# Kernel tuning notes

Measured on AMD Instinct MI355X. Metric: run time of the kernel, lower is better.

The kernel has to match this reference:

```python
import jax, jax.numpy as jnp
import numpy as np

GAMMA = 0.99
GAE_LAMBDA = 0.95
CLIP = 0.2
ENT_COEF = 0.01
VF_COEF = 0.5


def setup_inputs() -> dict:
    key = jax.random.key(0)
    ks = jax.random.split(key, 12)
    T, D, H, A = 65536, 512, 256, 16
    obs = jax.random.normal(ks[0], (T, D), dtype=jnp.float32)
    actions = jax.random.randint(ks[1], (T,), 0, A, dtype=jnp.int32)
    logprobs = jax.random.normal(ks[2], (T,), dtype=jnp.float32)
    rewards = jax.random.normal(ks[3], (T,), dtype=jnp.float32)
    terms = jax.random.uniform(ks[4], (T,), dtype=jnp.float32)
    values = jax.random.normal(ks[5], (T,), dtype=jnp.float32)
    # orthogonal-init-like scaling (std sqrt(2) for trunk, 0.01 actor, 1.0 critic)
    W1 = jax.random.normal(ks[6], (D, H), dtype=jnp.float32) * np.float32(np.sqrt(2.0 / D))
    b1 = jnp.zeros((H,), jnp.float32)
    W2 = jax.random.normal(ks[7], (H, H), dtype=jnp.float32) * np.float32(np.sqrt(2.0 / H))
    b2 = jnp.zeros((H,), jnp.float32)
    Wa = jax.random.normal(ks[8], (H, A), dtype=jnp.float32) * np.float32(0.01 / np.sqrt(H))
    ba = jnp.zeros((A,), jnp.float32)
    Wc = jax.random.normal(ks[9], (H, 1), dtype=jnp.float32) * np.float32(1.0 / np.sqrt(H))
    bc = jnp.zeros((1,), jnp.float32)
    return {"obs": obs, "actions": actions, "logprobs": logprobs, "rewards": rewards,
            "terms": terms, "values": values, "W1": W1, "b1": b1, "W2": W2, "b2": b2,
            "Wa": Wa, "ba": ba, "Wc": Wc, "bc": bc}


def reference(obs, actions, logprobs, rewards, terms, values,
              W1, b1, W2, b2, Wa, ba, Wc, bc):
    # ---- GAE (torch.no_grad in original -> stop_gradient) ----
    nonterm = 1.0 - terms                                   # [T]
    next_vals = jnp.concatenate([values[1:], jnp.zeros((1,), values.dtype)])
    delta = rewards + GAMMA * next_vals * nonterm - values  # [T]

    def step(carry, x):  # reverse recurrence a_t = d_t + g*l*nt_t * a_{t+1}
        d, nt = x
        g = d + GAMMA * GAE_LAMBDA * nt * carry
        return g, g

    _, adv = jax.lax.scan(step, jnp.float32(0.0), (delta, nonterm), reverse=True)
    adv = jax.lax.stop_gradient(adv)
    returns = adv + jax.lax.stop_gradient(values)
    vals_old = jax.lax.stop_gradient(values)

    # ---- actor-critic MLP (get_action_and_value) ----
    hidden = jnp.tanh(jnp.tanh(obs @ W1 + b1) @ W2 + b2)    # [T,256]
    logits = hidden @ Wa + ba                               # [T,A]
    logp = jax.nn.log_softmax(logits, axis=-1)
    newlp = jnp.take_along_axis(logp, actions[:, None].astype(jnp.int32), axis=1)[:, 0]
    entropy = -jnp.sum(jnp.exp(logp) * logp, axis=-1)       # [T]
    value = (hidden @ Wc + bc)[:, 0]                        # [T]

    # ---- clipped PPO losses (single full-batch minibatch) ----
    ratio = jnp.exp(newlp - logprobs)
    a = (adv - adv.mean()) / (adv.std() + 1e-8)
    pg_loss = jnp.maximum(-a * ratio, -a * jnp.clip(ratio, 1.0 - CLIP, 1.0 + CLIP)).mean()
    v_clipped = vals_old + jnp.clip(value - vals_old, -CLIP, CLIP)
    v_loss = 0.5 * jnp.maximum((value - returns) ** 2, (v_clipped - returns) ** 2).mean()
    loss = pg_loss - ENT_COEF * entropy.mean() + VF_COEF * v_loss
    return loss
```

## Files before the change

### kernel.cpp

```cpp
#include <hip/hip_runtime.h>


#define TT 65536

typedef float f32x4 __attribute__((ext_vector_type(4)));
typedef __bf16 bf16x8 __attribute__((ext_vector_type(8)));
typedef unsigned short u16x8 __attribute__((ext_vector_type(8)));
typedef unsigned int u32x4 __attribute__((ext_vector_type(4)));

__device__ __forceinline__ unsigned short f2bf(float f) {
    unsigned int u = __float_as_uint(f);
    unsigned int r = (u + 0x7fffu + ((u >> 16) & 1u)) >> 16;
    return (unsigned short)r;
}

__device__ __forceinline__ unsigned int cvt_pk_bf16(float a, float b) {
    unsigned int r;
    asm("v_cvt_pk_bf16_f32 %0, %1, %2" : "=v"(r) : "v"(a), "v"(b));
    return r;
}

__device__ __forceinline__ float fast_tanh(float x) {
    float e = __expf(2.0f * x);
    return fmaf(-2.0f, __builtin_amdgcn_rcpf(e + 1.0f), 1.0f);
}

__device__ __forceinline__ void lds_barrier() {
    asm volatile("s_waitcnt lgkmcnt(0)" ::: "memory");
    __builtin_amdgcn_s_barrier();
}

__device__ __forceinline__ void suffix_scan256(float* sC, float* sD, int i) {
    float c = sC[i], d = sD[i];
#pragma unroll
    for (int s = 1; s < 256; s <<= 1) {
        float c2 = 1.0f, d2 = 0.0f;
        if (i + s < 256) { c2 = sC[i + s]; d2 = sD[i + s]; }
        __syncthreads();
        d = d + c * d2;
        c = c * c2;
        sC[i] = c; sD[i] = d;
        __syncthreads();
    }
}

__device__ __forceinline__ void gae_cd(const float* rewards, const float* terms,
                                       const float* values, int t, float* c, float* d) {
    float nt = 1.0f - terms[t];
    float nv = (t + 1 < TT) ? values[t + 1] : 0.0f;
    *d = rewards[t] + 0.99f * nv * nt - values[t];
    *c = 0.99f * 0.95f * nt;
}

__global__ void k_prep_gae1(const float* __restrict__ W1, const float* __restrict__ W2,
                            const float* __restrict__ Wa, const float* __restrict__ Wc,
                            unsigned short* __restrict__ W1Tf, unsigned short* __restrict__ W2Tf,
                            unsigned short* __restrict__ Wavf,
                            const float* __restrict__ rewards, const float* __restrict__ terms,
                            const float* __restrict__ values, float* __restrict__ aggC,
                            float* __restrict__ aggD) {
    if (blockIdx.x < 800) {
        int idx = blockIdx.x * 256 + threadIdx.x;
        if (idx < 131072) {
            int col = idx & 255, k = idx >> 8;
            int kt = k >> 5, lh = (k & 31) >> 3, e = k & 7;
            int nt = col >> 4, cl = col & 15;
            W1Tf[(((kt * 16 + nt) * 64) + lh * 16 + cl) * 8 + e] = f2bf(W1[k * 256 + col]);
        } else if (idx < 196608) {
            int i = idx - 131072;
            int col = i & 255, k = i >> 8;
            int kt = k >> 5, lh = (k & 31) >> 3, e = k & 7;
            int nt = col >> 4, cl = col & 15;
            W2Tf[(((kt * 16 + nt) * 64) + lh * 16 + cl) * 8 + e] = f2bf(W2[k * 256 + col]);
        } else if (idx < 204800) {
            int i = idx - 196608;
            if (i < 4096) {
                int a = i & 15, k = i >> 4;
                int kt = k >> 5, lh = (k & 31) >> 3, e = k & 7;
                Wavf[(((kt * 2 + 0) * 64) + lh * 16 + a) * 8 + e] = f2bf(Wa[k * 16 + a]);
            } else {
                int j = i - 4096;
                int a = j & 15, k = j >> 4;
                int kt = k >> 5, lh = (k & 31) >> 3, e = k & 7;
                float v = (a == 0) ? Wc[k] : 0.0f;
                Wavf[(((kt * 2 + 1) * 64) + lh * 16 + a) * 8 + e] = f2bf(v);
            }
        }
        return;
    }
    __shared__ float sC[256], sD[256];
    int i = threadIdx.x;
    int b = blockIdx.x - 800;
    int t = b * 256 + i;
    float c, d;
    gae_cd(rewards, terms, values, t, &c, &d);
    sC[i] = c; sD[i] = d;
    __syncthreads();
    suffix_scan256(sC, sD, i);
    if (i == 0) { aggC[b] = sC[0]; aggD[b] = sD[0]; }
}

__global__ void k_gae3(const float* __restrict__ rewards, const float* __restrict__ terms,
                       const float* __restrict__ values, const float* __restrict__ aggC,
                       const float* __restrict__ aggD, float* __restrict__ adv,
                       float* __restrict__ ret, float* __restrict__ sumP) {
    __shared__ float sC[256], sD[256];
    int i = threadIdx.x, b = blockIdx.x;
    sC[i] = aggC[i]; sD[i] = aggD[i];
    __syncthreads();
    suffix_scan256(sC, sD, i);
    float carry = (b < 255) ? sD[b + 1] : 0.0f;
    __syncthreads();

    int t = b * 256 + i;
    float c, d;
    gae_cd(rewards, terms, values, t, &c, &d);
    sC[i] = c; sD[i] = d;
    __syncthreads();
    suffix_scan256(sC, sD, i);
    float a = sD[i] + sC[i] * carry;
    adv[t] = a;
    ret[t] = a + values[t];
    __syncthreads();
    sC[i] = a; sD[i] = a * a;
    __syncthreads();
#pragma unroll
    for (int s = 128; s > 0; s >>= 1) {
        if (i < s) { sC[i] += sC[i + s]; sD[i] += sD[i + s]; }
        __syncthreads();
    }
    if (i == 0) { sumP[2 * b] = sC[0]; sumP[2 * b + 1] = sD[0]; }
}

__global__ __launch_bounds__(256, 2) void k_mlp(
    const float* __restrict__ obs, const int* __restrict__ actions,
    const float* __restrict__ logprobs, const float* __restrict__ values,
    const float* __restrict__ b1, const float* __restrict__ b2,
    const float* __restrict__ ba, const float* __restrict__ bc,
    const unsigned short* __restrict__ W1Tf, const unsigned short* __restrict__ W2Tf,
    const unsigned short* __restrict__ Wavf, const float* __restrict__ adv,
    const float* __restrict__ ret, const float* __restrict__ sumP,
    float* __restrict__ lossP) {
    __shared__ __align__(16) unsigned char SM[65536];
    unsigned short* smA = (unsigned short*)SM;
    unsigned short* smH = (unsigned short*)SM;

    const int tid = threadIdx.x;
    const int wid = tid >> 6;
    const int lane = tid & 63;
    const int cl = lane & 15;
    const int gg = lane >> 4;
    const int bm0 = blockIdx.x * 64;

    float meanA, rstdA;
    {
        float* red = (float*)SM;
        red[tid] = sumP[2 * tid];
        red[256 + tid] = sumP[2 * tid + 1];
        __syncthreads();
#pragma unroll
        for (int s = 128; s > 0; s >>= 1) {
            if (tid < s) { red[tid] += red[tid + s]; red[256 + tid] += red[256 + tid + s]; }
            __syncthreads();
        }
        meanA = red[0] * (1.0f / TT);
        float var = red[256] * (1.0f / TT) - meanA * meanA;
        rstdA = 1.0f / (sqrtf(fmaxf(var, 0.0f)) + 1e-8f);
        __syncthreads();
    }

    float b1v[4], b2v[4];
#pragma unroll
    for (int n = 0; n < 4; ++n) {
        int c = wid * 64 + n * 16 + cl;
        b1v[n] = b1[c];
        b2v[n] = b2[c];
    }
    const float bav = ba[cl];
    const float bc0 = bc[0];

    {
        const int arow = tid >> 2;
        const int acl4 = (tid & 3) * 8;
        const int axor = (arow & 7) << 3;
        const float* aSrc = obs + (size_t)(bm0 + arow) * 512 + acl4;
        unsigned short* aDst = smA + arow * 512;
#pragma unroll
        for (int ct = 0; ct < 16; ++ct) {
            float4 f0 = *(const float4*)(aSrc + ct * 32);
            float4 f1 = *(const float4*)(aSrc + ct * 32 + 4);
            u32x4 pk;
            pk[0] = cvt_pk_bf16(f0.x, f0.y);
            pk[1] = cvt_pk_bf16(f0.z, f0.w);
            pk[2] = cvt_pk_bf16(f1.x, f1.y);
            pk[3] = cvt_pk_bf16(f1.z, f1.w);
            *(u32x4*)&aDst[(ct * 32 + acl4) ^ axor] = pk;
        }
    }

    f32x4 acc[4][4];
#pragma unroll
    for (int m = 0; m < 4; ++m)
#pragma unroll
        for (int n = 0; n < 4; ++n) acc[m][n] = (f32x4){0.f, 0.f, 0.f, 0.f};

    const unsigned short* b1Base = W1Tf + ((size_t)(wid * 4) << 9) + lane * 8;
    bf16x8 bv0[4];
#pragma unroll
    for (int n = 0; n < 4; ++n)
        bv0[n] = *(const bf16x8*)(b1Base + ((size_t)n << 9));

    lds_barrier();

#pragma unroll
    for (int t = 0; t < 16; ++t) {
        bf16x8 av[4], bv[4];
#pragma unroll
        for (int n = 0; n < 4; ++n)
            bv[n] = (t == 0) ? bv0[n]
                             : *(const bf16x8*)(b1Base + ((size_t)(t * 16 + n) << 9));
#pragma unroll
        for (int m = 0; m < 4; ++m) {
            int ra = m * 16 + cl;
            av[m] = *(const bf16x8*)&smA[ra * 512 + ((t * 32 + gg * 8) ^ ((ra & 7) << 3))];
        }
#pragma unroll
        for (int m = 0; m < 4; ++m)
#pragma unroll
            for (int n = 0; n < 4; ++n)
                acc[m][n] = __builtin_amdgcn_mfma_f32_16x16x32_bf16(av[m], bv[n], acc[m][n], 0, 0, 0);
    }

    const unsigned short* b2Base = W2Tf + ((size_t)(wid * 4) << 9) + lane * 8;
#pragma unroll
    for (int n = 0; n < 4; ++n)
        bv0[n] = *(const bf16x8*)(b2Base + ((size_t)n << 9));

    lds_barrier();

#pragma unroll
    for (int m = 0; m < 4; ++m)
#pragma unroll
        for (int n = 0; n < 4; ++n)
#pragma unroll
            for (int j = 0; j < 4; ++j) {
                int r = m * 16 + gg * 4 + j;
                int c = wid * 64 + n * 16 + cl;
                smH[r * 256 + (c ^ ((r & 7) << 3))] = f2bf(fast_tanh(acc[m][n][j] + b1v[n]));
                acc[m][n][j] = 0.0f;
            }
    lds_barrier();

#pragma unroll
    for (int t = 0; t < 8; ++t) {
        bf16x8 av[4], bv[4];
#pragma unroll
        for (int n = 0; n < 4; ++n)
            bv[n] = (t == 0) ? bv0[n]
                             : *(const bf16x8*)(b2Base + ((size_t)(t * 16 + n) << 9));
#pragma unroll
        for (int m = 0; m < 4; ++m) {
            int ra = m * 16 + cl;
            av[m] = *(const bf16x8*)&smH[ra * 256 + ((t * 32 + gg * 8) ^ ((ra & 7) << 3))];
        }
#pragma unroll
        for (int m = 0; m < 4; ++m)
#pragma unroll
            for (int n = 0; n < 4; ++n)
                acc[m][n] = __builtin_amdgcn_mfma_f32_16x16x32_bf16(av[m], bv[n], acc[m][n], 0, 0, 0);
    }

    lds_barrier();

#pragma unroll
    for (int m = 0; m < 4; ++m)
#pragma unroll
        for (int n = 0; n < 4; ++n)
#pragma unroll
            for (int j = 0; j < 4; ++j) {
                int r = m * 16 + gg * 4 + j;
                int c = wid * 64 + n * 16 + cl;
                smH[r * 256 + (c ^ ((r & 7) << 3))] = f2bf(fast_tanh(acc[m][n][j] + b2v[n]));
            }
    lds_barrier();

    float lsum = 0.0f;
    {
        f32x4 acc_a = {0.f, 0.f, 0.f, 0.f}, acc_v = {0.f, 0.f, 0.f, 0.f};
        const unsigned short* wBase = Wavf + lane * 8;
#pragma unroll
        for (int kk = 0; kk < 8; ++kk) {
            int r = wid * 16 + cl;
            bf16x8 av = *(const bf16x8*)&smH[r * 256 + ((kk * 32 + gg * 8) ^ ((r & 7) << 3))];
            bf16x8 bva = *(const bf16x8*)(wBase + ((size_t)(kk * 2) << 9));
            bf16x8 bvv = *(const bf16x8*)(wBase + ((size_t)(kk * 2 + 1) << 9));
            acc_a = __builtin_amdgcn_mfma_f32_16x16x32_bf16(av, bva, acc_a, 0, 0, 0);
            acc_v = __builtin_amdgcn_mfma_f32_16x16x32_bf16(av, bvv, acc_v, 0, 0, 0);
        }

        const int t0 = bm0 + wid * 16;
#pragma unroll
        for (int j = 0; j < 4; ++j) {
            int t = t0 + gg * 4 + j;
            float lg = acc_a[j] + bav;
            float mx = lg;
#pragma unroll
            for (int dd = 1; dd < 16; dd <<= 1) mx = fmaxf(mx, __shfl_xor(mx, dd));
            float ex = __expf(lg - mx);
            float se = ex;
#pragma unroll
            for (int dd = 1; dd < 16; dd <<= 1) se += __shfl_xor(se, dd);
            float ls = __logf(se);
            float lp = lg - mx - ls;
            float pl = __expf(lp) * lp;
            float ent = pl;
#pragma unroll
            for (int dd = 1; dd < 16; dd <<= 1) ent += __shfl_xor(ent, dd);
            ent = -ent;
            int act = actions[t];
            float newlp = __shfl(lp, (lane & 48) | act);
            float val = __shfl(acc_v[j], lane & 48) + bc0;

            float lpo = logprobs[t];
            float at = (adv[t] - meanA) * rstdA;
            float rt = ret[t];
            float vo = values[t];
            float ratio = __expf(newlp - lpo);
            float rcl = fminf(fmaxf(ratio, 0.8f), 1.2f);
            float pg = fmaxf(-at * ratio, -at * rcl);
            float vcl = vo + fminf(fmaxf(val - vo, -0.2f), 0.2f);
            float dv = val - rt, dvc = vcl - rt;
            float vl = fmaxf(dv * dv, dvc * dvc);
            if (cl == 0) lsum += pg - 0.01f * ent + 0.25f * vl;
        }
        lsum += __shfl_xor(lsum, 16);
        lsum += __shfl_xor(lsum, 32);
    }
    lds_barrier();
    float* red2 = (float*)SM;
    if (lane == 0) red2[wid] = lsum;
    lds_barrier();
    if (tid == 0) lossP[blockIdx.x] = red2[0] + red2[1] + red2[2] + red2[3];
}

__global__ void k_final(const float* __restrict__ lossP, float* __restrict__ out) {
    __shared__ float s[256];
    int i = threadIdx.x;
    s[i] = lossP[i] + lossP[i + 256] + lossP[i + 512] + lossP[i + 768];
    __syncthreads();
#pragma unroll
    for (int st = 128; st > 0; st >>= 1) {
        if (i < st) s[i] += s[i + st];
        __syncthreads();
    }
    if (i == 0) out[0] = s[0] * (1.0f / TT);
}

extern "C" void kernel_launch(void* const* d_in, const int* in_sizes, int n_in,
                              void* d_out, int out_size, void* d_ws, size_t ws_size,
                              hipStream_t stream) {
    const float* obs      = (const float*)d_in[0];
    const int*   actions  = (const int*)d_in[1];
    const float* logprobs = (const float*)d_in[2];
    const float* rewards  = (const float*)d_in[3];
    const float* terms    = (const float*)d_in[4];
    const float* values   = (const float*)d_in[5];
    const float* W1 = (const float*)d_in[6];
    const float* b1 = (const float*)d_in[7];
    const float* W2 = (const float*)d_in[8];
    const float* b2 = (const float*)d_in[9];
    const float* Wa = (const float*)d_in[10];
    const float* ba = (const float*)d_in[11];
    const float* Wc = (const float*)d_in[12];
    const float* bc = (const float*)d_in[13];

    char* ws = (char*)d_ws;
    unsigned short* W1Tf = (unsigned short*)(ws + 0);
    unsigned short* W2Tf = (unsigned short*)(ws + 262144);
    unsigned short* Wavf = (unsigned short*)(ws + 393216);
    float* advp  = (float*)(ws + 409600);
    float* retp  = (float*)(ws + 671744);
    float* aggC  = (float*)(ws + 933888);
    float* aggD  = (float*)(ws + 934912);
    float* sumP  = (float*)(ws + 936960);
    float* lossP = (float*)(ws + 939072);

    k_prep_gae1<<<1056, 256, 0, stream>>>(W1, W2, Wa, Wc, W1Tf, W2Tf, Wavf,
                                          rewards, terms, values, aggC, aggD);
    k_gae3<<<256, 256, 0, stream>>>(rewards, terms, values, aggC, aggD, advp, retp, sumP);
    k_mlp<<<1024, 256, 0, stream>>>(obs, actions, logprobs, values, b1, b2, ba, bc,
                                    W1Tf, W2Tf, Wavf, advp, retp, sumP, lossP);
    k_final<<<1, 256, 0, stream>>>(lossP, (float*)d_out);
}
```

Before: 67.35 us.

## Enlarge MLP tile to 128 rows and stream obs through double-buffered LDS

The MLP kernel now uses 512-thread blocks covering 128 rows each. Each of the 8 waves owns 32 output columns across 8 row tiles, so every weight fragment fetched is reused over twice as many rows. Instead of converting the whole 64x512 obs tile into LDS before the first GEMM, obs is loaded in 32-column K-chunks into a double-buffered LDS area, and the next chunk's global loads overlap the current chunk's MFMAs. The cost is a block-wide barrier per K step, and half as many blocks, which may reduce latency hiding on the CUs.

```diff
diff --git a/kernel.cpp b/kernel.cpp
--- a/kernel.cpp
+++ b/kernel.cpp
@@ -23,11 +23,6 @@
 __device__ __forceinline__ float fast_tanh(float x) {
     float e = __expf(2.0f * x);
     return fmaf(-2.0f, __builtin_amdgcn_rcpf(e + 1.0f), 1.0f);
-}
-
-__device__ __forceinline__ void lds_barrier() {
-    asm volatile("s_waitcnt lgkmcnt(0)" ::: "memory");
-    __builtin_amdgcn_s_barrier();
 }
 
 __device__ __forceinline__ void suffix_scan256(float* sC, float* sD, int i) {
@@ -132,7 +127,7 @@
     if (i == 0) { sumP[2 * b] = sC[0]; sumP[2 * b + 1] = sD[0]; }
 }
 
-__global__ __launch_bounds__(256, 2) void k_mlp(
+__global__ __launch_bounds__(512, 2) void k_mlp(
     const float* __restrict__ obs, const int* __restrict__ actions,
     const float* __restrict__ logprobs, const float* __restrict__ values,
     const float* __restrict__ b1, const float* __restrict__ b2,
@@ -150,13 +145,12 @@
     const int lane = tid & 63;
     const int cl = lane & 15;
     const int gg = lane >> 4;
-    const int bm0 = blockIdx.x * 64;
+    const int bm0 = blockIdx.x * 128;
 
     float meanA, rstdA;
     {
         float* red = (float*)SM;
-        red[tid] = sumP[2 * tid];
-        red[256 + tid] = sumP[2 * tid + 1];
+        if (tid < 256) { red[tid] = sumP[2 * tid]; red[256 + tid] = sumP[2 * tid + 1]; }
         __syncthreads();
 #pragma unroll
         for (int s = 128; s > 0; s >>= 1) {
@@ -169,120 +163,114 @@
         __syncthreads();
     }
 
-    float b1v[4], b2v[4];
-#pragma unroll
-    for (int n = 0; n < 4; ++n) {
-        int c = wid * 64 + n * 16 + cl;
+    float b1v[2], b2v[2];
+#pragma unroll
+    for (int n = 0; n < 2; ++n) {
+        int c = wid * 32 + n * 16 + cl;
         b1v[n] = b1[c];
         b2v[n] = b2[c];
     }
     const float bav = ba[cl];
     const float bc0 = bc[0];
 
+    const int arow = tid >> 2;
+    const int aslot = tid & 3;
+    const int adst = arow * 32 + ((aslot ^ ((arow >> 1) & 3)) << 3);
+    const float* aSrc = obs + (size_t)(bm0 + arow) * 512 + aslot * 8;
+
+    f32x4 acc[8][2];
+#pragma unroll
+    for (int m = 0; m < 8; ++m)
+#pragma unroll
+        for (int n = 0; n < 2; ++n) acc[m][n] = (f32x4){0.f, 0.f, 0.f, 0.f};
+
+    auto cvtWriteA = [&](const float4& f0, const float4& f1, int buf) {
+        u32x4 pk;
+        pk[0] = cvt_pk_bf16(f0.x, f0.y);
+        pk[1] = cvt_pk_bf16(f0.z, f0.w);
+        pk[2] = cvt_pk_bf16(f1.x, f1.y);
+        pk[3] = cvt_pk_bf16(f1.z, f1.w);
+        *(u32x4*)&smA[buf * 4096 + adst] = pk;
+    };
+
     {
-        const int arow = tid >> 2;
-        const int acl4 = (tid & 3) * 8;
-        const int axor = (arow & 7) << 3;
-        const float* aSrc = obs + (size_t)(bm0 + arow) * 512 + acl4;
-        unsigned short* aDst = smA + arow * 512;
-#pragma unroll
-        for (int ct = 0; ct < 16; ++ct) {
-            float4 f0 = *(const float4*)(aSrc + ct * 32);
-            float4 f1 = *(const float4*)(aSrc + ct * 32 + 4);
-            u32x4 pk;
-            pk[0] = cvt_pk_bf16(f0.x, f0.y);
-            pk[1] = cvt_pk_bf16(f0.z, f0.w);
-            pk[2] = cvt_pk_bf16(f1.x, f1.y);
-            pk[3] = cvt_pk_bf16(f1.z, f1.w);
-            *(u32x4*)&aDst[(ct * 32 + acl4) ^ axor] = pk;
-        }
-    }
-
-    f32x4 acc[4][4];
-#pragma unroll
-    for (int m = 0; m < 4; ++m)
-#pragma unroll
-        for (int n = 0; n < 4; ++n) acc[m][n] = (f32x4){0.f, 0.f, 0.f, 0.f};
-
-    const unsigned short* b1Base = W1Tf + ((size_t)(wid * 4) << 9) + lane * 8;
-    bf16x8 bv0[4];
-#pragma unroll
-    for (int n = 0; n < 4; ++n)
-        bv0[n] = *(const bf16x8*)(b1Base + ((size_t)n << 9));
-
-    lds_barrier();
-
-#pragma unroll
-    for (int t = 0; t < 16; ++t) {
-        bf16x8 av[4], bv[4];
-#pragma unroll
-        for (int n = 0; n < 4; ++n)
-            bv[n] = (t == 0) ? bv0[n]
-                             : *(const bf16x8*)(b1Base + ((size_t)(t * 16 + n) << 9));
-#pragma unroll
-        for (int m = 0; m < 4; ++m) {
-            int ra = m * 16 + cl;
-            av[m] = *(const bf16x8*)&smA[ra * 512 + ((t * 32 + gg * 8) ^ ((ra & 7) << 3))];
-        }
-#pragma unroll
-        for (int m = 0; m < 4; ++m)
-#pragma unroll
-            for (int n = 0; n < 4; ++n)
-                acc[m][n] = __builtin_amdgcn_mfma_f32_16x16x32_bf16(av[m], bv[n], acc[m][n], 0, 0, 0);
-    }
-
-    const unsigned short* b2Base = W2Tf + ((size_t)(wid * 4) << 9) + lane * 8;
-#pragma unroll
-    for (int n = 0; n < 4; ++n)
-        bv0[n] = *(const bf16x8*)(b2Base + ((size_t)n << 9));
-
-    lds_barrier();
-
-#pragma unroll
-    for (int m = 0; m < 4; ++m)
-#pragma unroll
-        for (int n = 0; n < 4; ++n)
+        const unsigned short* bBase = W1Tf + ((size_t)(wid * 2) << 9) + lane * 8;
+        float4 a0 = *(const float4*)(aSrc);
+        float4 a1 = *(const float4*)(aSrc + 4);
+        cvtWriteA(a0, a1, 0);
+        __syncthreads();
+#pragma unroll
+        for (int t = 0; t < 16; ++t) {
+            if (t < 15) {
+                a0 = *(const float4*)(aSrc + (t + 1) * 32);
+                a1 = *(const float4*)(aSrc + (t + 1) * 32 + 4);
+            }
+            bf16x8 av[8], bv[2];
+#pragma unroll
+            for (int n = 0; n < 2; ++n)
+                bv[n] = *(const bf16x8*)(bBase + ((size_t)(t * 16 + n) << 9));
+#pragma unroll
+            for (int m = 0; m < 8; ++m) {
+                int ra = m * 16 + cl;
+                av[m] = *(const bf16x8*)&smA[(t & 1) * 4096 + ra * 32 + ((gg ^ ((ra >> 1) & 3)) << 3)];
+            }
+#pragma unroll
+            for (int m = 0; m < 8; ++m)
+#pragma unroll
+                for (int n = 0; n < 2; ++n)
+                    acc[m][n] = __builtin_amdgcn_mfma_f32_16x16x32_bf16(av[m], bv[n], acc[m][n], 0, 0, 0);
+            if (t < 15) cvtWriteA(a0, a1, (t + 1) & 1);
+            __syncthreads();
+        }
+    }
+
+#pragma unroll
+    for (int m = 0; m < 8; ++m)
+#pragma unroll
+        for (int n = 0; n < 2; ++n)
 #pragma unroll
             for (int j = 0; j < 4; ++j) {
                 int r = m * 16 + gg * 4 + j;
-                int c = wid * 64 + n * 16 + cl;
+                int c = wid * 32 + n * 16 + cl;
                 smH[r * 256 + (c ^ ((r & 7) << 3))] = f2bf(fast_tanh(acc[m][n][j] + b1v[n]));
                 acc[m][n][j] = 0.0f;
             }
-    lds_barrier();
-
-#pragma unroll
-    for (int t = 0; t < 8; ++t) {
-        bf16x8 av[4], bv[4];
-#pragma unroll
-        for (int n = 0; n < 4; ++n)
-            bv[n] = (t == 0) ? bv0[n]
-                             : *(const bf16x8*)(b2Base + ((size_t)(t * 16 + n) << 9));
-#pragma unroll
-        for (int m = 0; m < 4; ++m) {
-            int ra = m * 16 + cl;
-            av[m] = *(const bf16x8*)&smH[ra * 256 + ((t * 32 + gg * 8) ^ ((ra & 7) << 3))];
-        }
-#pragma unroll
-        for (int m = 0; m < 4; ++m)
-#pragma unroll
-            for (int n = 0; n < 4; ++n)
-                acc[m][n] = __builtin_amdgcn_mfma_f32_16x16x32_bf16(av[m], bv[n], acc[m][n], 0, 0, 0);
-    }
-
-    lds_barrier();
-
-#pragma unroll
-    for (int m = 0; m < 4; ++m)
-#pragma unroll
-        for (int n = 0; n < 4; ++n)
+    __syncthreads();
+
+    {
+        const unsigned short* bBase = W2Tf + ((size_t)(wid * 2) << 9) + lane * 8;
+#pragma unroll
+        for (int t = 0; t < 8; ++t) {
+            bf16x8 av[8], bv[2];
+#pragma unroll
+            for (int n = 0; n < 2; ++n)
+                bv[n] = *(const bf16x8*)(bBase + ((size_t)(t * 16 + n) << 9));
+#pragma unroll
+            for (int m = 0; m < 8; ++m) {
+                int ra = m * 16 + cl;
+                av[m] = *(const bf16x8*)&smH[ra * 256 + ((t * 32 + gg * 8) ^ ((ra & 7) << 3))];
+            }
+#pragma unroll
+            for (int m = 0; m < 8; ++m)
+#pragma unroll
+                for (int n = 0; n < 2; ++n)
+                    acc[m][n] = __builtin_amdgcn_mfma_f32_16x16x32_bf16(av[m], bv[n], acc[m][n], 0, 0, 0);
+        }
+    }
+
+    __syncthreads();
+
+#pragma unroll
+    for (int m = 0; m < 8; ++m)
+#pragma unroll
+        for (int n = 0; n < 2; ++n)
 #pragma unroll
             for (int j = 0; j < 4; ++j) {
                 int r = m * 16 + gg * 4 + j;
-                int c = wid * 64 + n * 16 + cl;
+                int c = wid * 32 + n * 16 + cl;
                 smH[r * 256 + (c ^ ((r & 7) << 3))] = f2bf(fast_tanh(acc[m][n][j] + b2v[n]));
             }
-    lds_barrier();
+    __syncthreads();
 
     float lsum = 0.0f;
     {
@@ -336,17 +324,22 @@
         lsum += __shfl_xor(lsum, 16);
         lsum += __shfl_xor(lsum, 32);
     }
-    lds_barrier();
+    __syncthreads();
     float* red2 = (float*)SM;
     if (lane == 0) red2[wid] = lsum;
-    lds_barrier();
-    if (tid == 0) lossP[blockIdx.x] = red2[0] + red2[1] + red2[2] + red2[3];
+    __syncthreads();
+    if (tid == 0) {
+        float s = 0.0f;
+#pragma unroll
+        for (int w = 0; w < 8; ++w) s += red2[w];
+        lossP[blockIdx.x] = s;
+    }
 }
 
 __global__ void k_final(const float* __restrict__ lossP, float* __restrict__ out) {
     __shared__ float s[256];
     int i = threadIdx.x;
-    s[i] = lossP[i] + lossP[i + 256] + lossP[i + 512] + lossP[i + 768];
+    s[i] = lossP[i] + lossP[i + 256];
     __syncthreads();
 #pragma unroll
     for (int st = 128; st > 0; st >>= 1) {
@@ -388,7 +381,7 @@
     k_prep_gae1<<<1056, 256, 0, stream>>>(W1, W2, Wa, Wc, W1Tf, W2Tf, Wavf,
                                           rewards, terms, values, aggC, aggD);
     k_gae3<<<256, 256, 0, stream>>>(rewards, terms, values, aggC, aggD, advp, retp, sumP);
-    k_mlp<<<1024, 256, 0, stream>>>(obs, actions, logprobs, values, b1, b2, ba, bc,
-                                    W1Tf, W2Tf, Wavf, advp, retp, sumP, lossP);
+    k_mlp<<<512, 512, 0, stream>>>(obs, actions, logprobs, values, b1, b2, ba, bc,
+                                   W1Tf, W2Tf, Wavf, advp, retp, sumP, lossP);
     k_final<<<1, 256, 0, stream>>>(lossP, (float*)d_out);
 }
```

Result: slower. 76.37 us (+13.4%).
